# Optimization experiments

Hardware: AMD Instinct MI355X
Metric: run time of the kernel (lower is better)

## Reference

```python
import jax, jax.numpy as jnp
import numpy as np

FEATURES = 1024
EXPANDED = 16
HIDDEN = FEATURES * EXPANDED  # 16384
BATCH = 4096


def setup_inputs() -> dict:
    key = jax.random.key(0)
    k_x, k_we, k_be, k_wd, k_bd = jax.random.split(key, 5)
    s_enc = 1.0 / np.sqrt(FEATURES)
    s_dec = 1.0 / np.sqrt(HIDDEN)
    return {
        "x": jax.random.normal(k_x, (BATCH, FEATURES), dtype=jnp.float32),
        "W_enc": jax.random.uniform(k_we, (HIDDEN, FEATURES), jnp.float32, -s_enc, s_enc),
        "b_enc": jax.random.uniform(k_be, (HIDDEN,), jnp.float32, -s_enc, s_enc),
        "W_dec": jax.random.uniform(k_wd, (FEATURES, HIDDEN), jnp.float32, -s_dec, s_dec),
        "b_dec": jax.random.uniform(k_bd, (FEATURES,), jnp.float32, -s_dec, s_dec),
        "activate": 64,
    }


def reference(x, W_enc, b_enc, W_dec, b_dec, activate):
    # Encoder: subtract decoder bias, dense GEMM -> pre-activations a [B, HIDDEN]
    xbar = x - b_dec
    a = jnp.einsum("bf,hf->bh", xbar, W_enc) + b_enc
    # TopK per row, relu values, scatter back into a zero tensor
    vals, idx = jax.lax.top_k(a, activate)           # [B, k]
    f = jnp.zeros_like(a)
    rows = jnp.arange(a.shape[0])[:, None]           # [B, 1]
    f = f.at[rows, idx].set(jax.nn.relu(vals))
    # Decoder: dense GEMM back to feature space (faithful to original dense decode)
    xhat = jnp.einsum("bh,fh->bf", f, W_dec) + b_dec
    return f, xhat
```

## Files before the change

kernel.cpp:

```cpp
#include <hip/hip_runtime.h>
#include <cstdint>

#define B_ 4096
#define F_ 1024
#define H_ 16384
#define TOPK 64
#define MAXC 192
#define TWOE 0.020f

typedef unsigned short u16;
typedef __attribute__((ext_vector_type(8))) _Float16 f16x8;
typedef __attribute__((ext_vector_type(8))) unsigned short u16x8;
typedef __attribute__((ext_vector_type(4))) float f32x4;

__device__ __forceinline__ u16 f2bf(float f) {
  union { float f; uint32_t u; } v; v.f = f;
  uint32_t u = v.u;
  uint32_t r = u + 0x7FFFu + ((u >> 16) & 1u);
  return (u16)(r >> 16);
}
__device__ __forceinline__ float bf2f(u16 h) {
  union { uint32_t u; float f; } v; v.u = ((uint32_t)h) << 16; return v.f;
}
__device__ __forceinline__ u16 f2h(float f) {
  union { _Float16 h; u16 u; } v; v.h = (_Float16)f; return v.u;
}
__device__ __forceinline__ float h2f(u16 h) {
  union { _Float16 h; u16 u; } v; v.u = h; return (float)v.h;
}
__device__ __forceinline__ uint32_t key2(uint32_t v) {
  uint32_t s = (v >> 15) & 0x00010001u;
  return v & ~(s * 0xFFFFu);
}

__device__ __forceinline__ void async16(const void* g, void* l) {
  __builtin_amdgcn_global_load_lds(
      reinterpret_cast<const __attribute__((address_space(1))) uint32_t*>(
          reinterpret_cast<uintptr_t>(g)),
      reinterpret_cast<__attribute__((address_space(3))) uint32_t*>(
          reinterpret_cast<uintptr_t>(l)),
      16, 0, 0);
}

__global__ __launch_bounds__(256) void k_xbar(const float* __restrict__ x,
                                              const float* __restrict__ b_dec,
                                              u16* __restrict__ xbar) {
  int i = blockIdx.x * 256 + threadIdx.x;
  int base = i * 4;
  int col = base & (F_ - 1);
  float4 xv = *(const float4*)(x + base);
  float4 bv = *(const float4*)(b_dec + col);
  ushort4 o;
  o.x = f2h(xv.x - bv.x); o.y = f2h(xv.y - bv.y);
  o.z = f2h(xv.z - bv.z); o.w = f2h(xv.w - bv.w);
  *(ushort4*)(xbar + base) = o;
}

__global__ __launch_bounds__(256) void k_cast(const float* __restrict__ src,
                                              u16* __restrict__ dst) {
  size_t base = (size_t)(blockIdx.x * 256 + threadIdx.x) * 4;
  float4 v = *(const float4*)(src + base);
  ushort4 o; o.x = f2h(v.x); o.y = f2h(v.y); o.z = f2h(v.z); o.w = f2h(v.w);
  *(ushort4*)(dst + base) = o;
}

__global__ __launch_bounds__(256) void k_transpose(const float* __restrict__ Wdec,
                                                   u16* __restrict__ WdecT) {
  __shared__ float tile[32][33];
  int hb = blockIdx.x * 32, fb = blockIdx.y * 32;
  int tx = threadIdx.x & 31, ty = threadIdx.x >> 5;
#pragma unroll
  for (int i = 0; i < 32; i += 8)
    tile[ty + i][tx] = Wdec[(size_t)(fb + ty + i) * H_ + hb + tx];
  __syncthreads();
#pragma unroll
  for (int i = 0; i < 32; i += 8)
    WdecT[(size_t)(hb + ty + i) * F_ + fb + tx] = f2bf(tile[tx][ty + i]);
}

__device__ __forceinline__ void gemm_step(const u16* __restrict__ bA,
                                          const u16* __restrict__ bB,
                                          int aoff, int boff, int kcp,
                                          f32x4 (&acc)[4][4]) {
  f16x8 av[4], bv[4];
#pragma unroll
  for (int i = 0; i < 4; ++i)
    av[i] = *(const f16x8*)&bA[(aoff + i * 16) * 32 + kcp];
#pragma unroll
  for (int j = 0; j < 4; ++j)
    bv[j] = *(const f16x8*)&bB[(boff + j * 16) * 32 + kcp];
#pragma unroll
  for (int i = 0; i < 4; ++i)
#pragma unroll
    for (int j = 0; j < 4; ++j)
      acc[i][j] = __builtin_amdgcn_mfma_f32_16x16x32_f16(av[i], bv[j], acc[i][j], 0, 0, 0);
}

__global__ __launch_bounds__(256) void k_gemm(const u16* __restrict__ A,
                                              const u16* __restrict__ Bm,
                                              const float* __restrict__ b_enc,
                                              u16* __restrict__ Cf16,
                                              float* __restrict__ fzero,
                                              int by0) {
  __shared__ u16 lA[2][128 * 32];
  __shared__ u16 lB[2][128 * 32];
  const int tid = threadIdx.x;
  const int lane = tid & 63, wave = tid >> 6;
  const int wm = wave >> 1, wn = wave & 1;
  const int bx = blockIdx.x, by = by0 + blockIdx.y;

  const int kcs = (tid & 3) ^ ((tid >> 3) & 3);
  const u16* gA0 = A + (size_t)(by * 128 + (tid >> 2)) * F_ + kcs * 8;
  const u16* gB0 = Bm + (size_t)(bx * 128 + (tid >> 2)) * F_ + kcs * 8;

#define STAGE(b_, k0_)                                       \
  {                                                          \
    async16(gA0 + (k0_), &lA[b_][tid * 8]);                  \
    async16(gA0 + 64 * F_ + (k0_), &lA[b_][tid * 8 + 2048]); \
    async16(gB0 + (k0_), &lB[b_][tid * 8]);                  \
    async16(gB0 + 64 * F_ + (k0_), &lB[b_][tid * 8 + 2048]); \
  }

  f32x4 acc[4][4] = {};
  const int lm = lane & 15;
  const int kcp = (((lane >> 4) ^ ((lm >> 1) & 3))) * 8;
  const int aoff = wm * 64 + lm, boff = wn * 64 + lm;

  STAGE(0, 0);
  __syncthreads();
  int cur = 0;
#pragma unroll 1
  for (int t = 0; t < 31; ++t) {
    STAGE(cur ^ 1, (t + 1) * 32);
    gemm_step(lA[cur], lB[cur], aoff, boff, kcp, acc);
    __syncthreads();
    cur ^= 1;
  }
  gemm_step(lA[cur], lB[cur], aoff, boff, kcp, acc);
#undef STAGE

  {
    const int bid = by * 128 + bx;
    float* zp = fzero + (size_t)bid * 8192 + tid * 4;
    const f32x4 z4 = {0.f, 0.f, 0.f, 0.f};
#pragma unroll
    for (int k = 0; k < 8; ++k)
      __builtin_nontemporal_store(z4, (f32x4*)(zp + k * 1024));
  }

#pragma unroll
  for (int i = 0; i < 4; ++i) {
    int rowg = by * 128 + wm * 64 + i * 16 + (lane >> 4) * 4;
#pragma unroll
    for (int j = 0; j < 4; ++j) {
      int colg = bx * 128 + wn * 64 + j * 16 + lm;
      float be = b_enc[colg];
      u16* cp = Cf16 + (size_t)rowg * H_ + colg;
#pragma unroll
      for (int r = 0; r < 4; ++r)
        cp[(size_t)r * H_] = f2h(acc[i][j][r] + be);
    }
  }
}

__global__ __launch_bounds__(256) void k_selref(const u16* __restrict__ af16,
                                                const float* __restrict__ x,
                                                const float* __restrict__ b_dec,
                                                const float* __restrict__ Wenc,
                                                const float* __restrict__ b_enc,
                                                int* __restrict__ decIdx,
                                                float* __restrict__ decVal) {
  const int row = blockIdx.x, tid = threadIdx.x;
  const int lane = tid & 63, wave = tid >> 6;
  __shared__ float wbuf[4][2][F_];
  __shared__ float xs[F_];
  __shared__ double vals[MAXC];
  __shared__ float bes[MAXC];
  __shared__ int idxs[MAXC];
  __shared__ int s_cnt8[2][4];
  __shared__ int s_sure, s_amb;

  if (tid == 0) { s_sure = 0; s_amb = 0; idxs[0] = 0; }
  for (int k = tid; k < F_; k += 256)
    xs[k] = x[(size_t)row * F_ + k] - b_dec[k];

  uint32_t pr[32];
  {
    const uint4* arow16 = (const uint4*)(af16 + (size_t)row * H_);
#pragma unroll
    for (int j = 0; j < 8; ++j) {
      uint4 v = arow16[tid + 256 * j];
      pr[j * 4 + 0] = key2(v.x);
      pr[j * 4 + 1] = key2(v.y);
      pr[j * 4 + 2] = key2(v.z);
      pr[j * 4 + 3] = key2(v.w);
    }
  }

  uint32_t lo = 0, hi = 0x7C00;
  int it = 0;
  while (hi - lo > 1) {
    const uint32_t mid = (lo + hi) >> 1;
    int c = 0;
#pragma unroll
    for (int r = 0; r < 32; ++r) {
      c += ((pr[r] & 0xFFFFu) >= mid);
      c += ((pr[r] >> 16) >= mid);
    }
#pragma unroll
    for (int off = 32; off > 0; off >>= 1) c += __shfl_xor(c, off);
    if (lane == 0) s_cnt8[it & 1][wave] = c;
    __syncthreads();
    const int* sc = s_cnt8[it & 1];
    const int tot = sc[0] + sc[1] + sc[2] + sc[3];
    if (tot >= TOPK) lo = mid; else hi = mid;
    ++it;
  }
  const float v64f = h2f((u16)lo);
  const float sc = v64f + TWOE;
  const float al = v64f - TWOE;

  int* dI = decIdx + row * TOPK;
  float* dV = decVal + row * TOPK;
#pragma unroll
  for (int j = 0; j < 8; ++j) {
#pragma unroll
    for (int w = 0; w < 4; ++w) {
      const uint32_t v = pr[j * 4 + w];
      const int ib = (tid + 256 * j) * 8 + w * 2;
      const float f0 = h2f((u16)(v & 0xFFFFu));
      const float f1 = h2f((u16)(v >> 16));
      if (f0 > sc) {
        int p = atomicAdd(&s_sure, 1);
        if (p < TOPK) { dI[p] = ib; dV[p] = f0 > 0.f ? f0 : 0.f; }
      } else if (f0 >= al) {
        int p = atomicAdd(&s_amb, 1);
        if (p < MAXC) idxs[p] = ib;
      }
      if (f1 > sc) {
        int p = atomicAdd(&s_sure, 1);
        if (p < TOPK) { dI[p] = ib + 1; dV[p] = f1 > 0.f ? f1 : 0.f; }
      } else if (f1 >= al) {
        int p = atomicAdd(&s_amb, 1);
        if (p < MAXC) idxs[p] = ib + 1;
      }
    }
  }
  __syncthreads();
  const int S = s_sure < TOPK ? s_sure : TOPK;
  const int cnt = s_amb < MAXC ? s_amb : MAXC;
  for (int c = tid; c < cnt; c += 256) bes[c] = b_enc[idxs[c]];
  __syncthreads();

  float xr[16];
#pragma unroll
  for (int ch = 0; ch < 4; ++ch)
#pragma unroll
    for (int j = 0; j < 4; ++j)
      xr[ch * 4 + j] = xs[ch * 256 + lane * 4 + j];

#define ISSUE_ROW(c_, b_)                                                  \
  {                                                                        \
    int cc_ = (c_) < cnt ? (c_) : 0;                                       \
    const float* src_ = Wenc + (size_t)idxs[cc_] * F_ + lane * 4;          \
    float* dst_ = &wbuf[wave][(b_)][lane * 4];                             \
    async16(src_ + 0, dst_ + 0);                                           \
    async16(src_ + 256, dst_ + 256);                                       \
    async16(src_ + 512, dst_ + 512);                                       \
    async16(src_ + 768, dst_ + 768);                                       \
  }

  const int nIter = (cnt - wave + 3) / 4;
  ISSUE_ROW(wave, 0);
  ISSUE_ROW(wave + 4, 1);

  for (int i = 0; i < nIter; ++i) {
    const int c = wave + i * 4;
    const int bsel = i & 1;
    asm volatile("s_waitcnt vmcnt(4)" ::: "memory");
    __builtin_amdgcn_sched_barrier(0);

    const float4* wr = (const float4*)wbuf[wave][bsel];
    double s = 0.0;
#pragma unroll
    for (int ch = 0; ch < 4; ++ch) {
      float4 wv = wr[ch * 64 + lane];
      s = fma((double)xr[ch * 4 + 0], (double)wv.x, s);
      s = fma((double)xr[ch * 4 + 1], (double)wv.y, s);
      s = fma((double)xr[ch * 4 + 2], (double)wv.z, s);
      s = fma((double)xr[ch * 4 + 3], (double)wv.w, s);
    }
    __builtin_amdgcn_sched_barrier(0);
    ISSUE_ROW(wave + (i + 2) * 4, bsel);

#pragma unroll
    for (int off = 32; off > 0; off >>= 1) s += __shfl_xor(s, off);
    if (lane == 0 && c < cnt) vals[c] = s + (double)bes[c];
  }
#undef ISSUE_ROW
  __syncthreads();

  const int Kp = TOPK - S;
  for (int c = tid; c < cnt; c += 256) {
    const double v = vals[c];
    const int h = idxs[c];
    int rank = 0;
    for (int o = 0; o < cnt; ++o) {
      double vo = vals[o];
      rank += (vo > v) || (vo == v && idxs[o] < h);
    }
    if (rank < Kp) {
      float fv = v > 0.0 ? (float)v : 0.0f;
      dI[S + rank] = h;
      dV[S + rank] = fv;
    }
  }
}

__global__ __launch_bounds__(256) void k_decode(const int* __restrict__ decIdx,
                                               const float* __restrict__ decVal,
                                               const u16* __restrict__ WdecT,
                                               const float* __restrict__ b_dec,
                                               float* __restrict__ f,
                                               float* __restrict__ xhat) {
  const int row = blockIdx.x, tid = threadIdx.x;
  __shared__ int sIdx[TOPK];
  __shared__ float sVal[TOPK];
  __shared__ float part[F_];
  if (tid < TOPK) {
    sIdx[tid] = decIdx[row * TOPK + tid] & (H_ - 1);
    sVal[tid] = decVal[row * TOPK + tid];
  }
  float* frow = f + (size_t)row * H_;
  if (row >= B_ / 2) {
    const f32x4 z4 = {0.f, 0.f, 0.f, 0.f};
    for (int i = tid; i < H_ / 4; i += 256)
      __builtin_nontemporal_store(z4, (f32x4*)frow + i);
  }
  __syncthreads();
  if (tid < TOPK) frow[sIdx[tid]] = sVal[tid];

  const int cb = (tid & 127) * 8;
  const int par = tid >> 7;
  float a[8] = {0.f, 0.f, 0.f, 0.f, 0.f, 0.f, 0.f, 0.f};
#pragma unroll 8
  for (int j2 = 0; j2 < TOPK / 2; ++j2) {
    const int j = j2 * 2 + par;
    const float v = sVal[j];
    const u16x8 w = *(const u16x8*)(WdecT + (size_t)sIdx[j] * F_ + cb);
#pragma unroll
    for (int k = 0; k < 8; ++k) a[k] += v * bf2f(w[k]);
  }
  if (par) {
#pragma unroll
    for (int k = 0; k < 8; ++k) part[cb + k] = a[k];
  }
  __syncthreads();
  if (!par) {
    float4 bd0 = *(const float4*)(b_dec + cb);
    float4 bd1 = *(const float4*)(b_dec + cb + 4);
    float4 o0, o1;
    o0.x = a[0] + part[cb + 0] + bd0.x;
    o0.y = a[1] + part[cb + 1] + bd0.y;
    o0.z = a[2] + part[cb + 2] + bd0.z;
    o0.w = a[3] + part[cb + 3] + bd0.w;
    o1.x = a[4] + part[cb + 4] + bd1.x;
    o1.y = a[5] + part[cb + 5] + bd1.y;
    o1.z = a[6] + part[cb + 6] + bd1.z;
    o1.w = a[7] + part[cb + 7] + bd1.w;
    float* xp = xhat + (size_t)row * F_ + cb;
    *(float4*)xp = o0;
    *(float4*)(xp + 4) = o1;
  }
}

extern "C" void kernel_launch(void* const* d_in, const int* in_sizes, int n_in,
                              void* d_out, int out_size, void* d_ws, size_t ws_size,
                              hipStream_t stream) {
  const float* x    = (const float*)d_in[0];
  const float* Wenc = (const float*)d_in[1];
  const float* benc = (const float*)d_in[2];
  const float* Wdec = (const float*)d_in[3];
  const float* bdec = (const float*)d_in[4];

  float* out  = (float*)d_out;
  float* f    = out;
  float* xhat = out + (size_t)B_ * H_;
  u16* af16 = (u16*)(f + (size_t)B_ * H_ / 2);

  char* ws = (char*)d_ws;
  u16*  xbar    = (u16*)ws;
  u16*  wencb   = (u16*)(ws + (size_t)(8)  * 1048576);
  u16*  wdecT   = (u16*)(ws + (size_t)(40) * 1048576);
  int*  decIdx  = (int*)(ws + (size_t)(76) * 1048576);
  float* decVal = (float*)(ws + (size_t)(77) * 1048576);

  k_xbar<<<B_ * F_ / 1024, 256, 0, stream>>>(x, bdec, xbar);
  k_cast<<<H_ * F_ / 1024, 256, 0, stream>>>(Wenc, wencb);
  k_transpose<<<dim3(H_ / 32, F_ / 32), 256, 0, stream>>>(Wdec, wdecT);
  k_gemm<<<dim3(H_ / 128, B_ / 256), 256, 0, stream>>>(xbar, wencb, benc, af16, f, 0);
  k_gemm<<<dim3(H_ / 128, B_ / 256), 256, 0, stream>>>(xbar, wencb, benc, af16, f, 16);
  k_selref<<<B_, 256, 0, stream>>>(af16, x, bdec, Wenc, benc, decIdx, decVal);
  k_decode<<<B_, 256, 0, stream>>>(decIdx, decVal, wdecT, bdec, f, xhat);
}
```

Measured before the change: 747.8 us.

## Fuse top-k selection with decode and move f zeroing out of encoder GEMM

Merges the selection/refinement kernel and the decode kernel into one per-row kernel, so the chosen indices and values stay in shared memory rather than being re-read from global memory. Zeroing of the first half of f moves from the GEMM epilogue into the fused kernel. A new small kernel zeroes and scatters the second half of f, which aliases the fp16 pre-activation buffer, after selection has read it. The two half-grid GEMM launches become a single launch. The fused kernel holds more state at once, which may lower occupancy, and the GEMM no longer overlaps its zero stores with compute.

Measured after the change: 728.6 us. 1.03x faster.

```diff
diff --git a/kernel.cpp b/kernel.cpp
--- a/kernel.cpp
+++ b/kernel.cpp
@@ -99,15 +99,13 @@
 __global__ __launch_bounds__(256) void k_gemm(const u16* __restrict__ A,
                                               const u16* __restrict__ Bm,
                                               const float* __restrict__ b_enc,
-                                              u16* __restrict__ Cf16,
-                                              float* __restrict__ fzero,
-                                              int by0) {
+                                              u16* __restrict__ Cf16) {
   __shared__ u16 lA[2][128 * 32];
   __shared__ u16 lB[2][128 * 32];
   const int tid = threadIdx.x;
   const int lane = tid & 63, wave = tid >> 6;
   const int wm = wave >> 1, wn = wave & 1;
-  const int bx = blockIdx.x, by = by0 + blockIdx.y;
+  const int bx = blockIdx.x, by = blockIdx.y;
 
   const int kcs = (tid & 3) ^ ((tid >> 3) & 3);
   const u16* gA0 = A + (size_t)(by * 128 + (tid >> 2)) * F_ + kcs * 8;
@@ -139,15 +137,6 @@
   gemm_step(lA[cur], lB[cur], aoff, boff, kcp, acc);
 #undef STAGE
 
-  {
-    const int bid = by * 128 + bx;
-    float* zp = fzero + (size_t)bid * 8192 + tid * 4;
-    const f32x4 z4 = {0.f, 0.f, 0.f, 0.f};
-#pragma unroll
-    for (int k = 0; k < 8; ++k)
-      __builtin_nontemporal_store(z4, (f32x4*)(zp + k * 1024));
-  }
-
 #pragma unroll
   for (int i = 0; i < 4; ++i) {
     int rowg = by * 128 + wm * 64 + i * 16 + (lane >> 4) * 4;
@@ -163,13 +152,16 @@
   }
 }
 
-__global__ __launch_bounds__(256) void k_selref(const u16* __restrict__ af16,
-                                                const float* __restrict__ x,
-                                                const float* __restrict__ b_dec,
-                                                const float* __restrict__ Wenc,
-                                                const float* __restrict__ b_enc,
-                                                int* __restrict__ decIdx,
-                                                float* __restrict__ decVal) {
+__global__ __launch_bounds__(256) void k_selrefdec(const u16* __restrict__ af16,
+                                                   const float* __restrict__ x,
+                                                   const float* __restrict__ b_dec,
+                                                   const float* __restrict__ Wenc,
+                                                   const float* __restrict__ b_enc,
+                                                   const u16* __restrict__ WdecT,
+                                                   float* __restrict__ f,
+                                                   float* __restrict__ xhat,
+                                                   int* __restrict__ decIdx,
+                                                   float* __restrict__ decVal) {
   const int row = blockIdx.x, tid = threadIdx.x;
   const int lane = tid & 63, wave = tid >> 6;
   __shared__ float wbuf[4][2][F_];
@@ -177,12 +169,22 @@
   __shared__ double vals[MAXC];
   __shared__ float bes[MAXC];
   __shared__ int idxs[MAXC];
+  __shared__ int fIdx[TOPK];
+  __shared__ float fVal[TOPK];
   __shared__ int s_cnt8[2][4];
   __shared__ int s_sure, s_amb;
 
   if (tid == 0) { s_sure = 0; s_amb = 0; idxs[0] = 0; }
+  if (tid < TOPK) { fIdx[tid] = 0; fVal[tid] = 0.f; }
   for (int k = tid; k < F_; k += 256)
     xs[k] = x[(size_t)row * F_ + k] - b_dec[k];
+
+  float* frow = f + (size_t)row * H_;
+  if (row < B_ / 2) {
+    const f32x4 z4 = {0.f, 0.f, 0.f, 0.f};
+    for (int i = tid; i < H_ / 4; i += 256)
+      __builtin_nontemporal_store(z4, (f32x4*)frow + i);
+  }
 
   uint32_t pr[32];
   {
@@ -211,8 +213,8 @@
     for (int off = 32; off > 0; off >>= 1) c += __shfl_xor(c, off);
     if (lane == 0) s_cnt8[it & 1][wave] = c;
     __syncthreads();
-    const int* sc = s_cnt8[it & 1];
-    const int tot = sc[0] + sc[1] + sc[2] + sc[3];
+    const int* scp = s_cnt8[it & 1];
+    const int tot = scp[0] + scp[1] + scp[2] + scp[3];
     if (tot >= TOPK) lo = mid; else hi = mid;
     ++it;
   }
@@ -220,8 +222,6 @@
   const float sc = v64f + TWOE;
   const float al = v64f - TWOE;
 
-  int* dI = decIdx + row * TOPK;
-  float* dV = decVal + row * TOPK;
 #pragma unroll
   for (int j = 0; j < 8; ++j) {
 #pragma unroll
@@ -232,14 +232,14 @@
       const float f1 = h2f((u16)(v >> 16));
       if (f0 > sc) {
         int p = atomicAdd(&s_sure, 1);
-        if (p < TOPK) { dI[p] = ib; dV[p] = f0 > 0.f ? f0 : 0.f; }
+        if (p < TOPK) { fIdx[p] = ib; fVal[p] = f0 > 0.f ? f0 : 0.f; }
       } else if (f0 >= al) {
         int p = atomicAdd(&s_amb, 1);
         if (p < MAXC) idxs[p] = ib;
       }
       if (f1 > sc) {
         int p = atomicAdd(&s_sure, 1);
-        if (p < TOPK) { dI[p] = ib + 1; dV[p] = f1 > 0.f ? f1 : 0.f; }
+        if (p < TOPK) { fIdx[p] = ib + 1; fVal[p] = f1 > 0.f ? f1 : 0.f; }
       } else if (f1 >= al) {
         int p = atomicAdd(&s_amb, 1);
         if (p < MAXC) idxs[p] = ib + 1;
@@ -311,34 +311,17 @@
     }
     if (rank < Kp) {
       float fv = v > 0.0 ? (float)v : 0.0f;
-      dI[S + rank] = h;
-      dV[S + rank] = fv;
-    }
-  }
-}
-
-__global__ __launch_bounds__(256) void k_decode(const int* __restrict__ decIdx,
-                                               const float* __restrict__ decVal,
-                                               const u16* __restrict__ WdecT,
-                                               const float* __restrict__ b_dec,
-                                               float* __restrict__ f,
-                                               float* __restrict__ xhat) {
-  const int row = blockIdx.x, tid = threadIdx.x;
-  __shared__ int sIdx[TOPK];
-  __shared__ float sVal[TOPK];
-  __shared__ float part[F_];
+      fIdx[S + rank] = h;
+      fVal[S + rank] = fv;
+    }
+  }
+  __syncthreads();
+
   if (tid < TOPK) {
-    sIdx[tid] = decIdx[row * TOPK + tid] & (H_ - 1);
-    sVal[tid] = decVal[row * TOPK + tid];
-  }
-  float* frow = f + (size_t)row * H_;
-  if (row >= B_ / 2) {
-    const f32x4 z4 = {0.f, 0.f, 0.f, 0.f};
-    for (int i = tid; i < H_ / 4; i += 256)
-      __builtin_nontemporal_store(z4, (f32x4*)frow + i);
-  }
-  __syncthreads();
-  if (tid < TOPK) frow[sIdx[tid]] = sVal[tid];
+    decIdx[row * TOPK + tid] = fIdx[tid];
+    decVal[row * TOPK + tid] = fVal[tid];
+    if (row < B_ / 2) frow[fIdx[tid] & (H_ - 1)] = fVal[tid];
+  }
 
   const int cb = (tid & 127) * 8;
   const int par = tid >> 7;
@@ -346,32 +329,45 @@
 #pragma unroll 8
   for (int j2 = 0; j2 < TOPK / 2; ++j2) {
     const int j = j2 * 2 + par;
-    const float v = sVal[j];
-    const u16x8 w = *(const u16x8*)(WdecT + (size_t)sIdx[j] * F_ + cb);
+    const float v = fVal[j];
+    const u16x8 w = *(const u16x8*)(WdecT + (size_t)(fIdx[j] & (H_ - 1)) * F_ + cb);
 #pragma unroll
     for (int k = 0; k < 8; ++k) a[k] += v * bf2f(w[k]);
   }
   if (par) {
 #pragma unroll
-    for (int k = 0; k < 8; ++k) part[cb + k] = a[k];
+    for (int k = 0; k < 8; ++k) xs[cb + k] = a[k];
   }
   __syncthreads();
   if (!par) {
     float4 bd0 = *(const float4*)(b_dec + cb);
     float4 bd1 = *(const float4*)(b_dec + cb + 4);
     float4 o0, o1;
-    o0.x = a[0] + part[cb + 0] + bd0.x;
-    o0.y = a[1] + part[cb + 1] + bd0.y;
-    o0.z = a[2] + part[cb + 2] + bd0.z;
-    o0.w = a[3] + part[cb + 3] + bd0.w;
-    o1.x = a[4] + part[cb + 4] + bd1.x;
-    o1.y = a[5] + part[cb + 5] + bd1.y;
-    o1.z = a[6] + part[cb + 6] + bd1.z;
-    o1.w = a[7] + part[cb + 7] + bd1.w;
+    o0.x = a[0] + xs[cb + 0] + bd0.x;
+    o0.y = a[1] + xs[cb + 1] + bd0.y;
+    o0.z = a[2] + xs[cb + 2] + bd0.z;
+    o0.w = a[3] + xs[cb + 3] + bd0.w;
+    o1.x = a[4] + xs[cb + 4] + bd1.x;
+    o1.y = a[5] + xs[cb + 5] + bd1.y;
+    o1.z = a[6] + xs[cb + 6] + bd1.z;
+    o1.w = a[7] + xs[cb + 7] + bd1.w;
     float* xp = xhat + (size_t)row * F_ + cb;
     *(float4*)xp = o0;
     *(float4*)(xp + 4) = o1;
   }
+}
+
+__global__ __launch_bounds__(256) void k_zs(const int* __restrict__ decIdx,
+                                            const float* __restrict__ decVal,
+                                            float* __restrict__ f) {
+  const int row = B_ / 2 + blockIdx.x, tid = threadIdx.x;
+  float* frow = f + (size_t)row * H_;
+  const f32x4 z4 = {0.f, 0.f, 0.f, 0.f};
+  for (int i = tid; i < H_ / 4; i += 256)
+    __builtin_nontemporal_store(z4, (f32x4*)frow + i);
+  __syncthreads();
+  if (tid < TOPK)
+    frow[decIdx[row * TOPK + tid] & (H_ - 1)] = decVal[row * TOPK + tid];
 }
 
 extern "C" void kernel_launch(void* const* d_in, const int* in_sizes, int n_in,
@@ -398,8 +394,8 @@
   k_xbar<<<B_ * F_ / 1024, 256, 0, stream>>>(x, bdec, xbar);
   k_cast<<<H_ * F_ / 1024, 256, 0, stream>>>(Wenc, wencb);
   k_transpose<<<dim3(H_ / 32, F_ / 32), 256, 0, stream>>>(Wdec, wdecT);
-  k_gemm<<<dim3(H_ / 128, B_ / 256), 256, 0, stream>>>(xbar, wencb, benc, af16, f, 0);
-  k_gemm<<<dim3(H_ / 128, B_ / 256), 256, 0, stream>>>(xbar, wencb, benc, af16, f, 16);
-  k_selref<<<B_, 256, 0, stream>>>(af16, x, bdec, Wenc, benc, decIdx, decVal);
-  k_decode<<<B_, 256, 0, stream>>>(decIdx, decVal, wdecT, bdec, f, xhat);
-}
+  k_gemm<<<dim3(H_ / 128, B_ / 128), 256, 0, stream>>>(xbar, wencb, benc, af16);
+  k_selrefdec<<<B_, 256, 0, stream>>>(af16, x, bdec, Wenc, benc, wdecT,
+                                      f, xhat, decIdx, decVal);
+  k_zs<<<B_ / 2, 256, 0, stream>>>(decIdx, decVal, f);
+}
```
